# Kernel tuning notes

Measured on AMD Instinct MI355X. Metric: run time of the kernel, lower is better.

Reference implementation:

```python
import jax, jax.numpy as jnp
import numpy as np

B, R, C, OUT, IN = 256, 1152, 10, 16, 8


def setup_inputs() -> dict:
    key = jax.random.key(0)
    kx, kw = jax.random.split(key)
    x = jax.random.normal(kx, (B, R, IN), dtype=jnp.float32)
    W = jax.random.normal(kw, (R, C, OUT, IN), dtype=jnp.float32)
    return {"x": x, "W": W}


def _squash(s):
    # s: [B, C, OUT]
    mag_sq = jnp.sum(s * s, axis=-1, keepdims=True)
    mag = jnp.sqrt(mag_sq + 1e-8)
    return mag_sq / (1.0 + mag_sq) * (s / (mag + 1e-8))


def reference(x, W):
    # u_hat[b,r,c,o] = sum_i W[r,c,o,i] * x[b,r,i]  (no explicit W.repeat)
    u_hat = jnp.einsum('rcoi,bri->brco', W, x)
    b_ij = jnp.zeros((B, R, C), dtype=u_hat.dtype)
    v_j = None
    for it in range(3):
        c_ij = jax.nn.softmax(b_ij, axis=2)              # [B,R,C]
        s_j = jnp.einsum('brc,brco->bco', c_ij, u_hat)   # [B,C,OUT]
        v_j = _squash(s_j)                               # [B,C,OUT]
        if it < 2:
            b_ij = b_ij + jnp.einsum('brco,bco->brc', u_hat, v_j)
    return v_j
```

## Files before the change

### kernel.cpp

```cpp
#include <hip/hip_runtime.h>
#include <math.h>


typedef _Float16 h2 __attribute__((ext_vector_type(2)));
typedef _Float16 h4 __attribute__((ext_vector_type(4)));

#if __has_builtin(__builtin_amdgcn_fdot2)
#define FDOT2(a, b, c) __builtin_amdgcn_fdot2((a), (b), (c), false)
#else
static __device__ __forceinline__ float FDOT2(h2 a, h2 b, float c) {
    return c + (float)a.x * (float)b.x + (float)a.y * (float)b.y;
}
#endif

static __device__ __forceinline__ h2 CVTPK(float a, float b) {
#if __has_builtin(__builtin_amdgcn_cvt_pkrtz)
    return __builtin_bit_cast(h2, __builtin_amdgcn_cvt_pkrtz(a, b));
#else
    h2 r; r.x = (_Float16)a; r.y = (_Float16)b; return r;
#endif
}

#if __has_builtin(__builtin_amdgcn_rcpf)
#define FRCP(x) __builtin_amdgcn_rcpf(x)
#else
#define FRCP(x) (1.0f / (x))
#endif

#define BCH2(u) __builtin_bit_cast(h2, (u))

template<int CTRL>
static __device__ __forceinline__ float dpp_xadd(float x) {
    const int t = __builtin_amdgcn_update_dpp(
        0, __builtin_bit_cast(int, x), CTRL, 0xF, 0xF, true);
    return x + __builtin_bit_cast(float, t);
}
static __device__ __forceinline__ float og_allsum(float l) {
    l = dpp_xadd<0xB1>(l);
    l = dpp_xadd<0x4E>(l);
    l = dpp_xadd<0x141>(l);
    return l;
}

namespace {
constexpr int Bdim = 256;
constexpr int Rdim = 1152;
constexpr int Cdim = 10;
constexpr int Odim = 16;
constexpr int Idim = 8;
constexpr int CO   = 160;

constexpr int Rpad  = 1280;
constexpr int RPC   = 4;
constexpr int NPAIR = 2;
constexpr int NQ    = 80;
constexpr int NSP   = 80;
constexpr int WROW  = Cdim * Odim * Idim;
}

__global__ __launch_bounds__(256)
void conv_w(const float* __restrict__ W, _Float16* __restrict__ W16)
{
    const int i = blockIdx.x * 256 + threadIdx.x;
    const int r = i / (WROW / 4);
    h4 o = { (_Float16)0.f, (_Float16)0.f, (_Float16)0.f, (_Float16)0.f };
    if (r < Rdim) {
        const float4 v = reinterpret_cast<const float4*>(W)[i];
        o = { (_Float16)v.x, (_Float16)v.y, (_Float16)v.z, (_Float16)v.w };
    }
    reinterpret_cast<h4*>(W16)[i] = o;
}

__device__ __forceinline__ void stagepair(const _Float16* __restrict__ src,
                                          _Float16* dst, int lane)
{
#pragma unroll
    for (int k = 0; k < 5; ++k) {
        const _Float16* s = src + (size_t)(k * 64 + lane) * 8;
        _Float16* d = dst + k * 512;
        __builtin_amdgcn_global_load_lds((const __attribute__((address_space(1))) void*)s,
                                         (__attribute__((address_space(3))) void*)d,
                                         16, 0, 0);
    }
}

template<bool FIRST>
__global__ __launch_bounds__(256)
void caps_iter(const float* __restrict__ xf, const _Float16* __restrict__ W16,
               const float* __restrict__ Vsum, float* __restrict__ s_part)
{
    __shared__ __align__(16) _Float16 Wst[4][2][2560];

    const int tid  = threadIdx.x;
    const int wv   = tid >> 6;
    const int lane = tid & 63;
    const int og   = lane & 7;
    const int bl   = lane >> 3;

    const int quad = blockIdx.x;
    const int bgrp = blockIdx.y;
    const int chunk = quad * 4 + wv;
    const int r0    = chunk * RPC;
    const int b0    = bgrp * 16 + bl;
    const int b1    = b0 + 8;

    float va0[Cdim], vb0[Cdim], va1[Cdim], vb1[Cdim];
    if constexpr (!FIRST) {
#pragma unroll
        for (int c = 0; c < Cdim; ++c) {
            const float2 p = *reinterpret_cast<const float2*>(
                Vsum + (size_t)b0 * CO + c * Odim + og * 2);
            va0[c] = p.x; vb0[c] = p.y;
            const float2 q = *reinterpret_cast<const float2*>(
                Vsum + (size_t)b1 * CO + c * Odim + og * 2);
            va1[c] = q.x; vb1[c] = q.y;
        }
    }

    float sA0[Cdim], sA1[Cdim], sB0[Cdim], sB1[Cdim];
#pragma unroll
    for (int c = 0; c < Cdim; ++c) { sA0[c]=0.f; sA1[c]=0.f; sB0[c]=0.f; sB1[c]=0.f; }

    const _Float16* Wr = W16 + (size_t)r0 * WROW;
    const float* xb0 = xf + (size_t)b0 * (Rdim * Idim);
    const float* xb1 = xf + (size_t)b1 * (Rdim * Idim);

    auto xoff = [&](int p) -> int {
        int r = r0 + p * 2;
        return (r > Rdim - 2 ? Rdim - 2 : r) * Idim;
    };

    stagepair(Wr, &Wst[wv][0][0], lane);
    float4 xc[8];
    {
        const int o0 = xoff(0);
        xc[0] = *reinterpret_cast<const float4*>(xb0 + o0);
        xc[1] = *reinterpret_cast<const float4*>(xb0 + o0 + 4);
        xc[2] = *reinterpret_cast<const float4*>(xb0 + o0 + 8);
        xc[3] = *reinterpret_cast<const float4*>(xb0 + o0 + 12);
        xc[4] = *reinterpret_cast<const float4*>(xb1 + o0);
        xc[5] = *reinterpret_cast<const float4*>(xb1 + o0 + 4);
        xc[6] = *reinterpret_cast<const float4*>(xb1 + o0 + 8);
        xc[7] = *reinterpret_cast<const float4*>(xb1 + o0 + 12);
    }

    for (int p = 0; p < NPAIR; ++p) {
        asm volatile("s_waitcnt vmcnt(8)" ::: "memory");

        const _Float16* stcur = &Wst[wv][p & 1][0];

        float4 xn[8];
        if (p + 1 < NPAIR) {
            stagepair(Wr + (size_t)(p + 1) * 2 * WROW, &Wst[wv][(p + 1) & 1][0], lane);
            const int o1 = xoff(p + 1);
            xn[0] = *reinterpret_cast<const float4*>(xb0 + o1);
            xn[1] = *reinterpret_cast<const float4*>(xb0 + o1 + 4);
            xn[2] = *reinterpret_cast<const float4*>(xb0 + o1 + 8);
            xn[3] = *reinterpret_cast<const float4*>(xb0 + o1 + 12);
            xn[4] = *reinterpret_cast<const float4*>(xb1 + o1);
            xn[5] = *reinterpret_cast<const float4*>(xb1 + o1 + 4);
            xn[6] = *reinterpret_cast<const float4*>(xb1 + o1 + 8);
            xn[7] = *reinterpret_cast<const float4*>(xb1 + o1 + 12);
        }

#pragma unroll
        for (int rl = 0; rl < 2; ++rl) {
            const float4 pa0 = xc[rl * 2 + 0], pa1 = xc[rl * 2 + 1];
            const float4 pb0 = xc[rl * 2 + 4], pb1 = xc[rl * 2 + 5];
            const h2 a0 = CVTPK(pa0.x, pa0.y), a1 = CVTPK(pa0.z, pa0.w);
            const h2 a2 = CVTPK(pa1.x, pa1.y), a3 = CVTPK(pa1.z, pa1.w);
            const h2 e0 = CVTPK(pb0.x, pb0.y), e1 = CVTPK(pb0.z, pb0.w);
            const h2 e2 = CVTPK(pb1.x, pb1.y), e3 = CVTPK(pb1.z, pb1.w);

            const _Float16* wbase = stcur + rl * WROW + og * 16;
            float uA0[Cdim], uA1[Cdim], uB0[Cdim], uB1[Cdim];
#pragma unroll
            for (int c = 0; c < Cdim; ++c) {
                const uint4* wp = reinterpret_cast<const uint4*>(wbase + c * (Odim * Idim));
                const uint4 w0 = wp[0], w1 = wp[1];
                float t;
                t = FDOT2(BCH2(w0.x), a0, 0.f);  t = FDOT2(BCH2(w0.y), a1, t);
                t = FDOT2(BCH2(w0.z), a2, t);    uA0[c] = FDOT2(BCH2(w0.w), a3, t);
                t = FDOT2(BCH2(w1.x), a0, 0.f);  t = FDOT2(BCH2(w1.y), a1, t);
                t = FDOT2(BCH2(w1.z), a2, t);    uA1[c] = FDOT2(BCH2(w1.w), a3, t);
                t = FDOT2(BCH2(w0.x), e0, 0.f);  t = FDOT2(BCH2(w0.y), e1, t);
                t = FDOT2(BCH2(w0.z), e2, t);    uB0[c] = FDOT2(BCH2(w0.w), e3, t);
                t = FDOT2(BCH2(w1.x), e0, 0.f);  t = FDOT2(BCH2(w1.y), e1, t);
                t = FDOT2(BCH2(w1.z), e2, t);    uB1[c] = FDOT2(BCH2(w1.w), e3, t);
            }

            if constexpr (FIRST) {
#pragma unroll
                for (int c = 0; c < Cdim; ++c) {
                    sA0[c] += 0.1f * uA0[c];  sA1[c] += 0.1f * uA1[c];
                    sB0[c] += 0.1f * uB0[c];  sB1[c] += 0.1f * uB1[c];
                }
            } else {
                float eA[Cdim], eB[Cdim];
                float sumA = 0.f, sumB = 0.f;
#pragma unroll
                for (int c = 0; c < Cdim; ++c) {
                    float lA = uA0[c] * va0[c] + uA1[c] * vb0[c];
                    lA = og_allsum(lA);
                    eA[c] = __expf(lA);  sumA += eA[c];
                    float lB = uB0[c] * va1[c] + uB1[c] * vb1[c];
                    lB = og_allsum(lB);
                    eB[c] = __expf(lB);  sumB += eB[c];
                }
                const float rA = FRCP(sumA), rB = FRCP(sumB);
#pragma unroll
                for (int c = 0; c < Cdim; ++c) {
                    const float cwA = eA[c] * rA;
                    sA0[c] += cwA * uA0[c];  sA1[c] += cwA * uA1[c];
                    const float cwB = eB[c] * rB;
                    sB0[c] += cwB * uB0[c];  sB1[c] += cwB * uB1[c];
                }
            }
        }

        if (p + 1 < NPAIR) {
#pragma unroll
            for (int q = 0; q < 8; ++q) xc[q] = xn[q];
        }
    }

    __syncthreads();
    float* red = reinterpret_cast<float*>(&Wst[0][0][0]);
    {
        float* p0 = red + (wv * 16 + bl) * CO + og * 2;
        float* p1 = red + (wv * 16 + bl + 8) * CO + og * 2;
#pragma unroll
        for (int c = 0; c < Cdim; ++c) {
            *reinterpret_cast<float2*>(p0 + c * Odim) = make_float2(sA0[c], sA1[c]);
            *reinterpret_cast<float2*>(p1 + c * Odim) = make_float2(sB0[c], sB1[c]);
        }
    }
    __syncthreads();
#pragma unroll
    for (int k = 0; k < 10; ++k) {
        const int j = k * 256 + tid;
        const float t = red[j] + red[j + 2560] + red[j + 5120] + red[j + 7680];
        const int b2 = j / CO;
        const int co = j - b2 * CO;
        s_part[((size_t)quad * Bdim + bgrp * 16 + b2) * CO + co] = t;
    }
}

template<int MODE>
__global__ __launch_bounds__(256)
void caps_reduce(const float* __restrict__ s_part, float* __restrict__ Vsum,
                 float* __restrict__ out)
{
    const int idx = blockIdx.x * 256 + threadIdx.x;
    float s = 0.f;
#pragma unroll 8
    for (int k = 0; k < NSP; ++k) s += s_part[(size_t)k * (Bdim * CO) + idx];

    float ssq = s * s;
    ssq += __shfl_xor(ssq, 1);
    ssq += __shfl_xor(ssq, 2);
    ssq += __shfl_xor(ssq, 4);
    ssq += __shfl_xor(ssq, 8);

    const float mag = sqrtf(ssq + 1e-8f);
    const float v = ssq / (1.f + ssq) * s / (mag + 1e-8f);

    if constexpr (MODE == 2) out[idx] = v;
    else if constexpr (MODE == 1) Vsum[idx] += v;
    else Vsum[idx] = v;
}

extern "C" void kernel_launch(void* const* d_in, const int* in_sizes, int n_in,
                              void* d_out, int out_size, void* d_ws, size_t ws_size,
                              hipStream_t stream)
{
    const float* x = (const float*)d_in[0];
    const float* W = (const float*)d_in[1];
    float* out = (float*)d_out;

    float* s_part = (float*)d_ws;
    float* Vsum   = s_part + (size_t)NSP * Bdim * CO;
    _Float16* W16 = (_Float16*)(Vsum + Bdim * CO);

    conv_w<<<dim3(1600), dim3(256), 0, stream>>>(W, W16);

    const dim3 gi(NQ, Bdim / 16);
    const dim3 bi(256);
    const dim3 gr((Bdim * CO) / 256);
    const dim3 br(256);

    caps_iter<true><<<gi, bi, 0, stream>>>(x, W16, Vsum, s_part);
    caps_reduce<0><<<gr, br, 0, stream>>>(s_part, Vsum, out);
    caps_iter<false><<<gi, bi, 0, stream>>>(x, W16, Vsum, s_part);
    caps_reduce<1><<<gr, br, 0, stream>>>(s_part, Vsum, out);
    caps_iter<false><<<gi, bi, 0, stream>>>(x, W16, Vsum, s_part);
    caps_reduce<2><<<gr, br, 0, stream>>>(s_part, Vsum, out);
}
```

Measured before the change: 98.03 us.

## Materialize fp16 u_hat once and reuse it in later routing passes

The first routing pass now writes the prediction vectors u_hat to a global workspace buffer as packed fp16. The two later passes become a new kernel that reads that buffer instead of recomputing u_hat from staged W and x with fdot2 math. This removes the repeated dot-product work and the W/x staging from two passes. In exchange it adds a roughly 125 MB global write followed by two full reads, and it lowers precision by rounding u_hat and v to fp16. It also needs a much larger workspace.

```diff
diff --git a/kernel.cpp b/kernel.cpp
--- a/kernel.cpp
+++ b/kernel.cpp
@@ -28,6 +28,7 @@
 #endif
 
 #define BCH2(u) __builtin_bit_cast(h2, (u))
+#define BCU(x)  __builtin_bit_cast(unsigned, (x))
 
 template<int CTRL>
 static __device__ __forceinline__ float dpp_xadd(float x) {
@@ -50,12 +51,11 @@
 constexpr int Idim = 8;
 constexpr int CO   = 160;
 
-constexpr int Rpad  = 1280;
-constexpr int RPC   = 4;
-constexpr int NPAIR = 2;
-constexpr int NQ    = 80;
-constexpr int NSP   = 80;
-constexpr int WROW  = Cdim * Odim * Idim;
+constexpr int Rpad = 1280;
+constexpr int RPC  = 4;
+constexpr int NQ   = 80;
+constexpr int NSP  = 80;
+constexpr int WROW = Cdim * Odim * Idim;
 }
 
 __global__ __launch_bounds__(256)
@@ -84,12 +84,11 @@
     }
 }
 
-template<bool FIRST>
 __global__ __launch_bounds__(256)
-void caps_iter(const float* __restrict__ xf, const _Float16* __restrict__ W16,
-               const float* __restrict__ Vsum, float* __restrict__ s_part)
-{
-    __shared__ __align__(16) _Float16 Wst[4][2][2560];
+void caps_first(const float* __restrict__ xf, const _Float16* __restrict__ W16,
+                uint4* __restrict__ U, float* __restrict__ s_part)
+{
+    __shared__ __align__(16) _Float16 Wst[4][RPC * WROW];
 
     const int tid  = threadIdx.x;
     const int wv   = tid >> 6;
@@ -104,128 +103,70 @@
     const int b0    = bgrp * 16 + bl;
     const int b1    = b0 + 8;
 
-    float va0[Cdim], vb0[Cdim], va1[Cdim], vb1[Cdim];
-    if constexpr (!FIRST) {
-#pragma unroll
-        for (int c = 0; c < Cdim; ++c) {
-            const float2 p = *reinterpret_cast<const float2*>(
-                Vsum + (size_t)b0 * CO + c * Odim + og * 2);
-            va0[c] = p.x; vb0[c] = p.y;
-            const float2 q = *reinterpret_cast<const float2*>(
-                Vsum + (size_t)b1 * CO + c * Odim + og * 2);
-            va1[c] = q.x; vb1[c] = q.y;
-        }
-    }
-
     float sA0[Cdim], sA1[Cdim], sB0[Cdim], sB1[Cdim];
 #pragma unroll
     for (int c = 0; c < Cdim; ++c) { sA0[c]=0.f; sA1[c]=0.f; sB0[c]=0.f; sB1[c]=0.f; }
 
     const _Float16* Wr = W16 + (size_t)r0 * WROW;
+    stagepair(Wr, &Wst[wv][0], lane);
+    stagepair(Wr + 2 * WROW, &Wst[wv][2 * WROW], lane);
+
     const float* xb0 = xf + (size_t)b0 * (Rdim * Idim);
     const float* xb1 = xf + (size_t)b1 * (Rdim * Idim);
-
-    auto xoff = [&](int p) -> int {
-        int r = r0 + p * 2;
-        return (r > Rdim - 2 ? Rdim - 2 : r) * Idim;
-    };
-
-    stagepair(Wr, &Wst[wv][0][0], lane);
-    float4 xc[8];
-    {
-        const int o0 = xoff(0);
-        xc[0] = *reinterpret_cast<const float4*>(xb0 + o0);
-        xc[1] = *reinterpret_cast<const float4*>(xb0 + o0 + 4);
-        xc[2] = *reinterpret_cast<const float4*>(xb0 + o0 + 8);
-        xc[3] = *reinterpret_cast<const float4*>(xb0 + o0 + 12);
-        xc[4] = *reinterpret_cast<const float4*>(xb1 + o0);
-        xc[5] = *reinterpret_cast<const float4*>(xb1 + o0 + 4);
-        xc[6] = *reinterpret_cast<const float4*>(xb1 + o0 + 8);
-        xc[7] = *reinterpret_cast<const float4*>(xb1 + o0 + 12);
-    }
-
-    for (int p = 0; p < NPAIR; ++p) {
-        asm volatile("s_waitcnt vmcnt(8)" ::: "memory");
-
-        const _Float16* stcur = &Wst[wv][p & 1][0];
-
-        float4 xn[8];
-        if (p + 1 < NPAIR) {
-            stagepair(Wr + (size_t)(p + 1) * 2 * WROW, &Wst[wv][(p + 1) & 1][0], lane);
-            const int o1 = xoff(p + 1);
-            xn[0] = *reinterpret_cast<const float4*>(xb0 + o1);
-            xn[1] = *reinterpret_cast<const float4*>(xb0 + o1 + 4);
-            xn[2] = *reinterpret_cast<const float4*>(xb0 + o1 + 8);
-            xn[3] = *reinterpret_cast<const float4*>(xb0 + o1 + 12);
-            xn[4] = *reinterpret_cast<const float4*>(xb1 + o1);
-            xn[5] = *reinterpret_cast<const float4*>(xb1 + o1 + 4);
-            xn[6] = *reinterpret_cast<const float4*>(xb1 + o1 + 8);
-            xn[7] = *reinterpret_cast<const float4*>(xb1 + o1 + 12);
-        }
-
-#pragma unroll
-        for (int rl = 0; rl < 2; ++rl) {
-            const float4 pa0 = xc[rl * 2 + 0], pa1 = xc[rl * 2 + 1];
-            const float4 pb0 = xc[rl * 2 + 4], pb1 = xc[rl * 2 + 5];
-            const h2 a0 = CVTPK(pa0.x, pa0.y), a1 = CVTPK(pa0.z, pa0.w);
-            const h2 a2 = CVTPK(pa1.x, pa1.y), a3 = CVTPK(pa1.z, pa1.w);
-            const h2 e0 = CVTPK(pb0.x, pb0.y), e1 = CVTPK(pb0.z, pb0.w);
-            const h2 e2 = CVTPK(pb1.x, pb1.y), e3 = CVTPK(pb1.z, pb1.w);
-
-            const _Float16* wbase = stcur + rl * WROW + og * 16;
-            float uA0[Cdim], uA1[Cdim], uB0[Cdim], uB1[Cdim];
-#pragma unroll
-            for (int c = 0; c < Cdim; ++c) {
-                const uint4* wp = reinterpret_cast<const uint4*>(wbase + c * (Odim * Idim));
-                const uint4 w0 = wp[0], w1 = wp[1];
-                float t;
-                t = FDOT2(BCH2(w0.x), a0, 0.f);  t = FDOT2(BCH2(w0.y), a1, t);
-                t = FDOT2(BCH2(w0.z), a2, t);    uA0[c] = FDOT2(BCH2(w0.w), a3, t);
-                t = FDOT2(BCH2(w1.x), a0, 0.f);  t = FDOT2(BCH2(w1.y), a1, t);
-                t = FDOT2(BCH2(w1.z), a2, t);    uA1[c] = FDOT2(BCH2(w1.w), a3, t);
-                t = FDOT2(BCH2(w0.x), e0, 0.f);  t = FDOT2(BCH2(w0.y), e1, t);
-                t = FDOT2(BCH2(w0.z), e2, t);    uB0[c] = FDOT2(BCH2(w0.w), e3, t);
-                t = FDOT2(BCH2(w1.x), e0, 0.f);  t = FDOT2(BCH2(w1.y), e1, t);
-                t = FDOT2(BCH2(w1.z), e2, t);    uB1[c] = FDOT2(BCH2(w1.w), e3, t);
-            }
-
-            if constexpr (FIRST) {
-#pragma unroll
-                for (int c = 0; c < Cdim; ++c) {
-                    sA0[c] += 0.1f * uA0[c];  sA1[c] += 0.1f * uA1[c];
-                    sB0[c] += 0.1f * uB0[c];  sB1[c] += 0.1f * uB1[c];
-                }
-            } else {
-                float eA[Cdim], eB[Cdim];
-                float sumA = 0.f, sumB = 0.f;
-#pragma unroll
-                for (int c = 0; c < Cdim; ++c) {
-                    float lA = uA0[c] * va0[c] + uA1[c] * vb0[c];
-                    lA = og_allsum(lA);
-                    eA[c] = __expf(lA);  sumA += eA[c];
-                    float lB = uB0[c] * va1[c] + uB1[c] * vb1[c];
-                    lB = og_allsum(lB);
-                    eB[c] = __expf(lB);  sumB += eB[c];
-                }
-                const float rA = FRCP(sumA), rB = FRCP(sumB);
-#pragma unroll
-                for (int c = 0; c < Cdim; ++c) {
-                    const float cwA = eA[c] * rA;
-                    sA0[c] += cwA * uA0[c];  sA1[c] += cwA * uA1[c];
-                    const float cwB = eB[c] * rB;
-                    sB0[c] += cwB * uB0[c];  sB1[c] += cwB * uB1[c];
-                }
-            }
-        }
-
-        if (p + 1 < NPAIR) {
-#pragma unroll
-            for (int q = 0; q < 8; ++q) xc[q] = xn[q];
-        }
+    float4 xc[4][4];
+#pragma unroll
+    for (int q = 0; q < 4; ++q) {
+        int r = r0 + q;
+        const int off = (r > Rdim - 1 ? Rdim - 1 : r) * Idim;
+        xc[q][0] = *reinterpret_cast<const float4*>(xb0 + off);
+        xc[q][1] = *reinterpret_cast<const float4*>(xb0 + off + 4);
+        xc[q][2] = *reinterpret_cast<const float4*>(xb1 + off);
+        xc[q][3] = *reinterpret_cast<const float4*>(xb1 + off + 4);
+    }
+    asm volatile("s_waitcnt vmcnt(0)" ::: "memory");
+
+#pragma unroll
+    for (int q = 0; q < 4; ++q) {
+        const int r = r0 + q;
+        const h2 a0 = CVTPK(xc[q][0].x, xc[q][0].y), a1 = CVTPK(xc[q][0].z, xc[q][0].w);
+        const h2 a2 = CVTPK(xc[q][1].x, xc[q][1].y), a3 = CVTPK(xc[q][1].z, xc[q][1].w);
+        const h2 e0 = CVTPK(xc[q][2].x, xc[q][2].y), e1 = CVTPK(xc[q][2].z, xc[q][2].w);
+        const h2 e2 = CVTPK(xc[q][3].x, xc[q][3].y), e3 = CVTPK(xc[q][3].z, xc[q][3].w);
+
+        const _Float16* wbase = &Wst[wv][q * WROW] + og * 16;
+        unsigned wA[Cdim], wB[Cdim];
+#pragma unroll
+        for (int c = 0; c < Cdim; ++c) {
+            const uint4* wp = reinterpret_cast<const uint4*>(wbase + c * (Odim * Idim));
+            const uint4 w0 = wp[0], w1 = wp[1];
+            float t;
+            float uA0, uA1, uB0, uB1;
+            t = FDOT2(BCH2(w0.x), a0, 0.f);  t = FDOT2(BCH2(w0.y), a1, t);
+            t = FDOT2(BCH2(w0.z), a2, t);    uA0 = FDOT2(BCH2(w0.w), a3, t);
+            t = FDOT2(BCH2(w1.x), a0, 0.f);  t = FDOT2(BCH2(w1.y), a1, t);
+            t = FDOT2(BCH2(w1.z), a2, t);    uA1 = FDOT2(BCH2(w1.w), a3, t);
+            t = FDOT2(BCH2(w0.x), e0, 0.f);  t = FDOT2(BCH2(w0.y), e1, t);
+            t = FDOT2(BCH2(w0.z), e2, t);    uB0 = FDOT2(BCH2(w0.w), e3, t);
+            t = FDOT2(BCH2(w1.x), e0, 0.f);  t = FDOT2(BCH2(w1.y), e1, t);
+            t = FDOT2(BCH2(w1.z), e2, t);    uB1 = FDOT2(BCH2(w1.w), e3, t);
+            sA0[c] += 0.1f * uA0;  sA1[c] += 0.1f * uA1;
+            sB0[c] += 0.1f * uB0;  sB1[c] += 0.1f * uB1;
+            wA[c] = BCU(CVTPK(uA0, uA1));
+            wB[c] = BCU(CVTPK(uB0, uB1));
+        }
+
+        uint4* Ua = U + (((size_t)r * Bdim + b0) * 3) * 8 + og;
+        uint4* Ub = U + (((size_t)r * Bdim + b1) * 3) * 8 + og;
+        Ua[0]  = make_uint4(wA[0], wA[1], wA[2], wA[3]);
+        Ua[8]  = make_uint4(wA[4], wA[5], wA[6], wA[7]);
+        Ua[16] = make_uint4(wA[8], wA[9], 0u, 0u);
+        Ub[0]  = make_uint4(wB[0], wB[1], wB[2], wB[3]);
+        Ub[8]  = make_uint4(wB[4], wB[5], wB[6], wB[7]);
+        Ub[16] = make_uint4(wB[8], wB[9], 0u, 0u);
     }
 
     __syncthreads();
-    float* red = reinterpret_cast<float*>(&Wst[0][0][0]);
+    float* red = reinterpret_cast<float*>(&Wst[0][0]);
     {
         float* p0 = red + (wv * 16 + bl) * CO + og * 2;
         float* p1 = red + (wv * 16 + bl + 8) * CO + og * 2;
@@ -246,6 +187,96 @@
     }
 }
 
+__global__ __launch_bounds__(256)
+void caps_pass(const uint4* __restrict__ U, const float* __restrict__ Vsum,
+               float* __restrict__ s_part)
+{
+    __shared__ __align__(16) float red[4 * 16 * CO];
+
+    const int tid  = threadIdx.x;
+    const int wv   = tid >> 6;
+    const int lane = tid & 63;
+    const int og   = lane & 7;
+    const int bl   = lane >> 3;
+
+    const int quad = blockIdx.x;
+    const int bgrp = blockIdx.y;
+    const int chunk = quad * 4 + wv;
+    const int r0    = chunk * RPC;
+    const int b0    = bgrp * 16 + bl;
+    const int b1    = b0 + 8;
+
+    h2 vh0[Cdim], vh1[Cdim];
+#pragma unroll
+    for (int c = 0; c < Cdim; ++c) {
+        const float2 p = *reinterpret_cast<const float2*>(
+            Vsum + (size_t)b0 * CO + c * Odim + og * 2);
+        vh0[c] = CVTPK(p.x, p.y);
+        const float2 q = *reinterpret_cast<const float2*>(
+            Vsum + (size_t)b1 * CO + c * Odim + og * 2);
+        vh1[c] = CVTPK(q.x, q.y);
+    }
+
+    float sA0[Cdim], sA1[Cdim], sB0[Cdim], sB1[Cdim];
+#pragma unroll
+    for (int c = 0; c < Cdim; ++c) { sA0[c]=0.f; sA1[c]=0.f; sB0[c]=0.f; sB1[c]=0.f; }
+
+#pragma unroll
+    for (int q = 0; q < RPC; ++q) {
+        const int r = r0 + q;
+        const uint4* Ua = U + (((size_t)r * Bdim + b0) * 3) * 8 + og;
+        const uint4* Ub = U + (((size_t)r * Bdim + b1) * 3) * 8 + og;
+        const uint4 qa0 = Ua[0], qa1 = Ua[8], qa2 = Ua[16];
+        const uint4 qb0 = Ub[0], qb1 = Ub[8], qb2 = Ub[16];
+        const unsigned wa[Cdim] = { qa0.x, qa0.y, qa0.z, qa0.w,
+                                    qa1.x, qa1.y, qa1.z, qa1.w, qa2.x, qa2.y };
+        const unsigned wb[Cdim] = { qb0.x, qb0.y, qb0.z, qb0.w,
+                                    qb1.x, qb1.y, qb1.z, qb1.w, qb2.x, qb2.y };
+
+        float eA[Cdim], eB[Cdim];
+        float sumA = 0.f, sumB = 0.f;
+#pragma unroll
+        for (int c = 0; c < Cdim; ++c) {
+            float lA = FDOT2(BCH2(wa[c]), vh0[c], 0.f);
+            lA = og_allsum(lA);
+            eA[c] = __expf(lA);  sumA += eA[c];
+            float lB = FDOT2(BCH2(wb[c]), vh1[c], 0.f);
+            lB = og_allsum(lB);
+            eB[c] = __expf(lB);  sumB += eB[c];
+        }
+        const float rA = FRCP(sumA), rB = FRCP(sumB);
+#pragma unroll
+        for (int c = 0; c < Cdim; ++c) {
+            const h2 ua = BCH2(wa[c]);
+            const h2 ub = BCH2(wb[c]);
+            const float cwA = eA[c] * rA;
+            sA0[c] += cwA * (float)ua.x;  sA1[c] += cwA * (float)ua.y;
+            const float cwB = eB[c] * rB;
+            sB0[c] += cwB * (float)ub.x;  sB1[c] += cwB * (float)ub.y;
+        }
+    }
+
+    __syncthreads();
+    {
+        float* p0 = red + (wv * 16 + bl) * CO + og * 2;
+        float* p1 = red + (wv * 16 + bl + 8) * CO + og * 2;
+#pragma unroll
+        for (int c = 0; c < Cdim; ++c) {
+            *reinterpret_cast<float2*>(p0 + c * Odim) = make_float2(sA0[c], sA1[c]);
+            *reinterpret_cast<float2*>(p1 + c * Odim) = make_float2(sB0[c], sB1[c]);
+        }
+    }
+    __syncthreads();
+#pragma unroll
+    for (int k = 0; k < 10; ++k) {
+        const int j = k * 256 + tid;
+        const float t = red[j] + red[j + 2560] + red[j + 5120] + red[j + 7680];
+        const int b2 = j / CO;
+        const int co = j - b2 * CO;
+        s_part[((size_t)quad * Bdim + bgrp * 16 + b2) * CO + co] = t;
+    }
+}
+
 template<int MODE>
 __global__ __launch_bounds__(256)
 void caps_reduce(const float* __restrict__ s_part, float* __restrict__ Vsum,
@@ -281,6 +312,7 @@
     float* s_part = (float*)d_ws;
     float* Vsum   = s_part + (size_t)NSP * Bdim * CO;
     _Float16* W16 = (_Float16*)(Vsum + Bdim * CO);
+    uint4* U      = (uint4*)(W16 + (size_t)Rpad * WROW);
 
     conv_w<<<dim3(1600), dim3(256), 0, stream>>>(W, W16);
 
@@ -289,10 +321,10 @@
     const dim3 gr((Bdim * CO) / 256);
     const dim3 br(256);
 
-    caps_iter<true><<<gi, bi, 0, stream>>>(x, W16, Vsum, s_part);
+    caps_first<<<gi, bi, 0, stream>>>(x, W16, U, s_part);
     caps_reduce<0><<<gr, br, 0, stream>>>(s_part, Vsum, out);
-    caps_iter<false><<<gi, bi, 0, stream>>>(x, W16, Vsum, s_part);
+    caps_pass<<<gi, bi, 0, stream>>>(U, Vsum, s_part);
     caps_reduce<1><<<gr, br, 0, stream>>>(s_part, Vsum, out);
-    caps_iter<false><<<gi, bi, 0, stream>>>(x, W16, Vsum, s_part);
+    caps_pass<<<gi, bi, 0, stream>>>(U, Vsum, s_part);
     caps_reduce<2><<<gr, br, 0, stream>>>(s_part, Vsum, out);
 }
```

New measurement: 99.88 us. About the same (+1.9%).
